# Optimization experiments

Hardware: AMD Instinct MI355X
Metric: run time of the kernel (lower is better)

The kernel has to match this reference:

```python
import jax, jax.numpy as jnp
import numpy as np

B, C, H, W = 4, 48, 512, 512

def gaussian_kernel(kernel_size, channels):
    # matches torch get_gaussian_kernel: sigma from OpenCV rule
    sigma = 0.3 * ((kernel_size - 1) * 0.5 - 1) + 0.8
    grid = np.arange(kernel_size, dtype=np.float32) - kernel_size // 2
    k1 = np.exp(-grid ** 2 / (2 * sigma ** 2))
    k1 /= k1.sum()
    k2 = np.outer(k1, k1)  # [k,k]
    # OIHW depthwise: [C, 1, k, k]
    return jnp.asarray(np.broadcast_to(k2, (channels, 1, kernel_size, kernel_size)))

def depthwise_conv(x, kernel, pad):
    # x: [B,C,H,W], kernel: [C,1,k,k]
    return jax.lax.conv_general_dilated(
        x, kernel,
        window_strides=(1, 1),
        padding=((pad, pad), (pad, pad)),
        dimension_numbers=('NCHW', 'OIHW', 'NCHW'),
        feature_group_count=x.shape[1])

def setup_inputs() -> dict:
    key = jax.random.key(0)
    s = jax.random.normal(key, (B, C, H, W), dtype=jnp.float32)
    one = jnp.ones((), dtype=jnp.float32)
    return {'s': s, 'w1': one, 'w2': one, 'w3': one, 'w4': one}

def reference(s, w1, w2, w3, w4):
    channels = s.shape[1]
    k3 = gaussian_kernel(3, channels)
    k5 = gaussian_kernel(5, channels)
    k7 = gaussian_kernel(7, channels)
    s3 = depthwise_conv(s, k3, 1)
    s5 = depthwise_conv(s, k5, 2)
    s7 = depthwise_conv(s, k7, 3)
    # fused diff + weighted sum: w1*s + w2*(s-s3) + w3*(s3-s5) + w4*(s5-s7)
    return w1 * s + w2 * (s - s3) + w3 * (s3 - s5) + w4 * (s5 - s7)
```

## Files before the change

### kernel.cpp

```cpp
#include <hip/hip_runtime.h>
#include <math.h>

#define STRIP_H 32

struct GaussCoefs { float g3[3]; float g5[5]; float g7[7]; };

__device__ __forceinline__ float rfl(float x) {
    return __int_as_float(__builtin_amdgcn_readfirstlane(__float_as_int(x)));
}

#define Z4 make_float4(0.f, 0.f, 0.f, 0.f)

#define ADD4(A, W, F) \
    A.x = fmaf((W), (F).x, A.x); A.y = fmaf((W), (F).y, A.y); \
    A.z = fmaf((W), (F).z, A.z); A.w = fmaf((W), (F).w, A.w);

#define DOT7(a,b,c,d,e,f,g) \
    fmaf(g7h0,(a), fmaf(g7h1,(b), fmaf(g7h2,(c), fmaf(g7h3,(d), \
    fmaf(g7h4,(e), fmaf(g7h5,(f), (g7h6)*(g)))))))
#define DOT5(a,b,c,d,e) \
    fmaf(g5h0,(a), fmaf(g5h1,(b), fmaf(g5h2,(c), fmaf(g5h3,(d), (g5h4)*(e)))))
#define DOT3(a,b,c) \
    fmaf(g3h0,(a), fmaf(g3h1,(b), (g3h2)*(c)))

#define LOADR(vA, vB, vC) \
    float4 vA, vB, vC; \
    if ((unsigned)row < (unsigned)Hd) { \
        const float* rp_ = sp + row * Wd; \
        vA = *(const float4*)(rp_ + offA); \
        vB = *(const float4*)(rp_ + offB); \
        vC = *(const float4*)(rp_ + offC); \
        if (killA) vA = Z4; \
        if (killC) vC = Z4; \
    } else { vA = Z4; vB = Z4; vC = Z4; } \
    ++row;

#define H7CALC(vA,vB,vC,h7) float4 h7; \
    h7.x = DOT7(vA.y,vA.z,vA.w,vB.x,vB.y,vB.z,vB.w); \
    h7.y = DOT7(vA.z,vA.w,vB.x,vB.y,vB.z,vB.w,vC.x); \
    h7.z = DOT7(vA.w,vB.x,vB.y,vB.z,vB.w,vC.x,vC.y); \
    h7.w = DOT7(vB.x,vB.y,vB.z,vB.w,vC.x,vC.y,vC.z);
#define H5CALC(vA,vB,vC,h5) float4 h5; \
    h5.x = DOT5(vA.z,vA.w,vB.x,vB.y,vB.z); \
    h5.y = DOT5(vA.w,vB.x,vB.y,vB.z,vB.w); \
    h5.z = DOT5(vB.x,vB.y,vB.z,vB.w,vC.x); \
    h5.w = DOT5(vB.y,vB.z,vB.w,vC.x,vC.y);
#define H3CALC(vA,vB,vC,h3) float4 h3; \
    h3.x = DOT3(vA.w,vB.x,vB.y); \
    h3.y = DOT3(vB.x,vB.y,vB.z); \
    h3.z = DOT3(vB.y,vB.z,vB.w); \
    h3.w = DOT3(vB.z,vB.w,vC.x);

#define MAINSTEP(S0,S1,S2,S3,S4,S5,S6) { \
    LOADR(vA, vB, vC); \
    H7CALC(vA,vB,vC,h7); H5CALC(vA,vB,vC,h5); H3CALC(vA,vB,vC,h3); \
    ADD4(S0, w7v6, h7); ADD4(S1, w7v5, h7); ADD4(S2, w7v4, h7); \
    ADD4(S3, w7v3, h7); ADD4(S4, w7v2, h7); ADD4(S5, w7v1, h7); \
    ADD4(S6, w7v0, h7); \
    ADD4(S1, w5v4, h5); ADD4(S2, w5v3, h5); ADD4(S3, w5v2, h5); \
    ADD4(S4, w5v1, h5); ADD4(S5, w5v0, h5); \
    ADD4(S2, w3v2, h3); ADD4(S3, w3v1, h3); ADD4(S4, w3v0, h3); \
    ADD4(S3, a0, vB); \
    *(float4*)(op + orow * Wd + xb) = S0; \
    S0 = Z4; ++orow; }

__global__ __launch_bounds__(256, 4) void mgdf_kernel(
    const float* __restrict__ s,
    const float* __restrict__ w1p, const float* __restrict__ w2p,
    const float* __restrict__ w3p, const float* __restrict__ w4p,
    float* __restrict__ out,
    GaussCoefs gc, int Wd, int Hd)
{
    const int tid  = threadIdx.x;
    const int lane = tid & 63;
    const int xh   = (tid >> 6) & 1;
    const int ysub = tid >> 7;
    const int plane = blockIdx.z;
    const int xb   = xh * 256 + lane * 4;
    const int ys0  = (blockIdx.y * 2 + ysub) * STRIP_H;

    const float* sp = s + (size_t)plane * Hd * Wd;
    float*       op = out + (size_t)plane * Hd * Wd;

    const float w1 = *w1p, w2 = *w2p, w3 = *w3p, w4 = *w4p;
    const float a0v = w1 + w2, a3v = w3 - w2, a5v = w4 - w3, a7v = -w4;

    const float g7h0 = gc.g7[0], g7h1 = gc.g7[1], g7h2 = gc.g7[2],
                g7h3 = gc.g7[3], g7h4 = gc.g7[4], g7h5 = gc.g7[5],
                g7h6 = gc.g7[6];
    const float g5h0 = gc.g5[0], g5h1 = gc.g5[1], g5h2 = gc.g5[2],
                g5h3 = gc.g5[3], g5h4 = gc.g5[4];
    const float g3h0 = gc.g3[0], g3h1 = gc.g3[1], g3h2 = gc.g3[2];

    const float a0   = rfl(a0v);
    const float w7v0 = rfl(a7v * g7h0), w7v1 = rfl(a7v * g7h1),
                w7v2 = rfl(a7v * g7h2), w7v3 = rfl(a7v * g7h3),
                w7v4 = rfl(a7v * g7h4), w7v5 = rfl(a7v * g7h5),
                w7v6 = rfl(a7v * g7h6);
    const float w5v0 = rfl(a5v * g5h0), w5v1 = rfl(a5v * g5h1),
                w5v2 = rfl(a5v * g5h2), w5v3 = rfl(a5v * g5h3),
                w5v4 = rfl(a5v * g5h4);
    const float w3v0 = rfl(a3v * g3h0), w3v1 = rfl(a3v * g3h1),
                w3v2 = rfl(a3v * g3h2);

    const bool killA = (xb - 4) < 0;
    const bool killC = (xb + 7) >= Wd;
    const int offA = killA ? xb : (xb - 4);
    const int offB = xb;
    const int offC = killC ? xb : (xb + 4);

    int row  = ys0 - 3;
    int orow = ys0;

    float4 A0 = Z4, A1 = Z4, A2 = Z4, A3 = Z4,
           A4 = Z4, A5 = Z4, A6 = Z4, A7 = Z4;

    { LOADR(vA,vB,vC); H7CALC(vA,vB,vC,h7);
      ADD4(A0, w7v0, h7); }
    { LOADR(vA,vB,vC); H7CALC(vA,vB,vC,h7); H5CALC(vA,vB,vC,h5);
      ADD4(A1, w7v0, h7); ADD4(A0, w7v1, h7);
      ADD4(A0, w5v0, h5); }
    { LOADR(vA,vB,vC); H7CALC(vA,vB,vC,h7); H5CALC(vA,vB,vC,h5); H3CALC(vA,vB,vC,h3);
      ADD4(A2, w7v0, h7); ADD4(A1, w7v1, h7); ADD4(A0, w7v2, h7);
      ADD4(A1, w5v0, h5); ADD4(A0, w5v1, h5);
      ADD4(A0, w3v0, h3); }
    { LOADR(vA,vB,vC); H7CALC(vA,vB,vC,h7); H5CALC(vA,vB,vC,h5); H3CALC(vA,vB,vC,h3);
      ADD4(A3, w7v0, h7); ADD4(A2, w7v1, h7); ADD4(A1, w7v2, h7); ADD4(A0, w7v3, h7);
      ADD4(A2, w5v0, h5); ADD4(A1, w5v1, h5); ADD4(A0, w5v2, h5);
      ADD4(A1, w3v0, h3); ADD4(A0, w3v1, h3);
      ADD4(A0, a0, vB); }
    { LOADR(vA,vB,vC); H7CALC(vA,vB,vC,h7); H5CALC(vA,vB,vC,h5); H3CALC(vA,vB,vC,h3);
      ADD4(A4, w7v0, h7); ADD4(A3, w7v1, h7); ADD4(A2, w7v2, h7);
      ADD4(A1, w7v3, h7); ADD4(A0, w7v4, h7);
      ADD4(A3, w5v0, h5); ADD4(A2, w5v1, h5); ADD4(A1, w5v2, h5); ADD4(A0, w5v3, h5);
      ADD4(A2, w3v0, h3); ADD4(A1, w3v1, h3); ADD4(A0, w3v2, h3);
      ADD4(A1, a0, vB); }
    { LOADR(vA,vB,vC); H7CALC(vA,vB,vC,h7); H5CALC(vA,vB,vC,h5); H3CALC(vA,vB,vC,h3);
      ADD4(A5, w7v0, h7); ADD4(A4, w7v1, h7); ADD4(A3, w7v2, h7);
      ADD4(A2, w7v3, h7); ADD4(A1, w7v4, h7); ADD4(A0, w7v5, h7);
      ADD4(A4, w5v0, h5); ADD4(A3, w5v1, h5); ADD4(A2, w5v2, h5);
      ADD4(A1, w5v3, h5); ADD4(A0, w5v4, h5);
      ADD4(A3, w3v0, h3); ADD4(A2, w3v1, h3); ADD4(A1, w3v2, h3);
      ADD4(A2, a0, vB); }

    #pragma unroll 1
    for (int it = 0; it < STRIP_H / 8; ++it) {
        MAINSTEP(A0, A1, A2, A3, A4, A5, A6);
        MAINSTEP(A1, A2, A3, A4, A5, A6, A7);
        MAINSTEP(A2, A3, A4, A5, A6, A7, A0);
        MAINSTEP(A3, A4, A5, A6, A7, A0, A1);
        MAINSTEP(A4, A5, A6, A7, A0, A1, A2);
        MAINSTEP(A5, A6, A7, A0, A1, A2, A3);
        MAINSTEP(A6, A7, A0, A1, A2, A3, A4);
        MAINSTEP(A7, A0, A1, A2, A3, A4, A5);
    }
}

static void fill_gauss(float* g, int k) {
    const double sigma = 0.3 * ((k - 1) * 0.5 - 1.0) + 0.8;
    double t[7], sum = 0.0;
    for (int i = 0; i < k; ++i) {
        const double x = (double)(i - k / 2);
        t[i] = exp(-x * x / (2.0 * sigma * sigma));
        sum += t[i];
    }
    for (int i = 0; i < k; ++i) g[i] = (float)(t[i] / sum);
}

extern "C" void kernel_launch(void* const* d_in, const int* in_sizes, int n_in,
                              void* d_out, int out_size, void* d_ws, size_t ws_size,
                              hipStream_t stream) {
    const float* s  = (const float*)d_in[0];
    const float* w1 = (const float*)d_in[1];
    const float* w2 = (const float*)d_in[2];
    const float* w3 = (const float*)d_in[3];
    const float* w4 = (const float*)d_in[4];
    float* out = (float*)d_out;

    const int Hd = 512, Wd = 512;
    const int planes = in_sizes[0] / (Hd * Wd);

    GaussCoefs gc;
    fill_gauss(gc.g3, 3);
    fill_gauss(gc.g5, 5);
    fill_gauss(gc.g7, 7);

    dim3 grid(1, Hd / (2 * STRIP_H), planes);
    mgdf_kernel<<<grid, 256, 0, stream>>>(s, w1, w2, w3, w4, out, gc, Wd, Hd);
}
```

Measured before the change: 370.2 us.

## Software-prefetch next row with double-buffered registers and halve strip height

Each step now issues the global loads for the next input row into a second set of registers before computing on the current row, so load latency can overlap with the filter arithmetic. The strip height is halved to 16 and the main loop is fully unrolled, which doubles the number of blocks and the share of halo rows reloaded per strip. The extra prefetch buffers raise register pressure under the 4-blocks-per-CU launch bound.

```diff
diff --git a/kernel.cpp b/kernel.cpp
--- a/kernel.cpp
+++ b/kernel.cpp
@@ -1,7 +1,7 @@
 #include <hip/hip_runtime.h>
 #include <math.h>
 
-#define STRIP_H 32
+#define STRIP_H 16
 
 struct GaussCoefs { float g3[3]; float g5[5]; float g7[7]; };
 
@@ -23,46 +23,64 @@
 #define DOT3(a,b,c) \
     fmaf(g3h0,(a), fmaf(g3h1,(b), (g3h2)*(c)))
 
-#define LOADR(vA, vB, vC) \
-    float4 vA, vB, vC; \
+#define PFLOAD(NA, NB, NC) \
     if ((unsigned)row < (unsigned)Hd) { \
-        const float* rp_ = sp + row * Wd; \
-        vA = *(const float4*)(rp_ + offA); \
-        vB = *(const float4*)(rp_ + offB); \
-        vC = *(const float4*)(rp_ + offC); \
-        if (killA) vA = Z4; \
-        if (killC) vC = Z4; \
-    } else { vA = Z4; vB = Z4; vC = Z4; } \
+        const float* rp_ = sp + (size_t)row * Wd; \
+        NA = *(const float4*)(rp_ + offA); \
+        NB = *(const float4*)(rp_ + offB); \
+        NC = *(const float4*)(rp_ + offC); \
+    } else { NA = Z4; NB = Z4; NC = Z4; } \
     ++row;
 
-#define H7CALC(vA,vB,vC,h7) float4 h7; \
-    h7.x = DOT7(vA.y,vA.z,vA.w,vB.x,vB.y,vB.z,vB.w); \
-    h7.y = DOT7(vA.z,vA.w,vB.x,vB.y,vB.z,vB.w,vC.x); \
-    h7.z = DOT7(vA.w,vB.x,vB.y,vB.z,vB.w,vC.x,vC.y); \
-    h7.w = DOT7(vB.x,vB.y,vB.z,vB.w,vC.x,vC.y,vC.z);
-#define H5CALC(vA,vB,vC,h5) float4 h5; \
-    h5.x = DOT5(vA.z,vA.w,vB.x,vB.y,vB.z); \
-    h5.y = DOT5(vA.w,vB.x,vB.y,vB.z,vB.w); \
-    h5.z = DOT5(vB.x,vB.y,vB.z,vB.w,vC.x); \
-    h5.w = DOT5(vB.y,vB.z,vB.w,vC.x,vC.y);
-#define H3CALC(vA,vB,vC,h3) float4 h3; \
-    h3.x = DOT3(vA.w,vB.x,vB.y); \
-    h3.y = DOT3(vB.x,vB.y,vB.z); \
-    h3.z = DOT3(vB.y,vB.z,vB.w); \
-    h3.w = DOT3(vB.z,vB.w,vC.x);
-
-#define MAINSTEP(S0,S1,S2,S3,S4,S5,S6) { \
-    LOADR(vA, vB, vC); \
-    H7CALC(vA,vB,vC,h7); H5CALC(vA,vB,vC,h5); H3CALC(vA,vB,vC,h3); \
+#define CSTEP(CA,CB,CC, NA,NB,NC, ...) { \
+    PFLOAD(NA, NB, NC); \
+    if (killA) CA = Z4; \
+    if (killC) CC = Z4; \
+    float4 h7, h5, h3; \
+    h7.x = DOT7(CA.y,CA.z,CA.w,CB.x,CB.y,CB.z,CB.w); \
+    h7.y = DOT7(CA.z,CA.w,CB.x,CB.y,CB.z,CB.w,CC.x); \
+    h7.z = DOT7(CA.w,CB.x,CB.y,CB.z,CB.w,CC.x,CC.y); \
+    h7.w = DOT7(CB.x,CB.y,CB.z,CB.w,CC.x,CC.y,CC.z); \
+    h5.x = DOT5(CA.z,CA.w,CB.x,CB.y,CB.z); \
+    h5.y = DOT5(CA.w,CB.x,CB.y,CB.z,CB.w); \
+    h5.z = DOT5(CB.x,CB.y,CB.z,CB.w,CC.x); \
+    h5.w = DOT5(CB.y,CB.z,CB.w,CC.x,CC.y); \
+    h3.x = DOT3(CA.w,CB.x,CB.y); \
+    h3.y = DOT3(CB.x,CB.y,CB.z); \
+    h3.z = DOT3(CB.y,CB.z,CB.w); \
+    h3.w = DOT3(CB.z,CB.w,CC.x); \
+    (void)h5; (void)h3; \
+    __VA_ARGS__ }
+
+#define CSTEP_LAST(CA,CB,CC, ...) { \
+    if (killA) CA = Z4; \
+    if (killC) CC = Z4; \
+    float4 h7, h5, h3; \
+    h7.x = DOT7(CA.y,CA.z,CA.w,CB.x,CB.y,CB.z,CB.w); \
+    h7.y = DOT7(CA.z,CA.w,CB.x,CB.y,CB.z,CB.w,CC.x); \
+    h7.z = DOT7(CA.w,CB.x,CB.y,CB.z,CB.w,CC.x,CC.y); \
+    h7.w = DOT7(CB.x,CB.y,CB.z,CB.w,CC.x,CC.y,CC.z); \
+    h5.x = DOT5(CA.z,CA.w,CB.x,CB.y,CB.z); \
+    h5.y = DOT5(CA.w,CB.x,CB.y,CB.z,CB.w); \
+    h5.z = DOT5(CB.x,CB.y,CB.z,CB.w,CC.x); \
+    h5.w = DOT5(CB.y,CB.z,CB.w,CC.x,CC.y); \
+    h3.x = DOT3(CA.w,CB.x,CB.y); \
+    h3.y = DOT3(CB.x,CB.y,CB.z); \
+    h3.z = DOT3(CB.y,CB.z,CB.w); \
+    h3.w = DOT3(CB.z,CB.w,CC.x); \
+    (void)h5; (void)h3; \
+    __VA_ARGS__ }
+
+#define MAINB(S0,S1,S2,S3,S4,S5,S6, CB) \
     ADD4(S0, w7v6, h7); ADD4(S1, w7v5, h7); ADD4(S2, w7v4, h7); \
     ADD4(S3, w7v3, h7); ADD4(S4, w7v2, h7); ADD4(S5, w7v1, h7); \
     ADD4(S6, w7v0, h7); \
     ADD4(S1, w5v4, h5); ADD4(S2, w5v3, h5); ADD4(S3, w5v2, h5); \
     ADD4(S4, w5v1, h5); ADD4(S5, w5v0, h5); \
     ADD4(S2, w3v2, h3); ADD4(S3, w3v1, h3); ADD4(S4, w3v0, h3); \
-    ADD4(S3, a0, vB); \
-    *(float4*)(op + orow * Wd + xb) = S0; \
-    S0 = Z4; ++orow; }
+    ADD4(S3, a0, CB); \
+    *(float4*)(op + (size_t)orow * Wd + xb) = S0; \
+    S0 = Z4; ++orow;
 
 __global__ __launch_bounds__(256, 4) void mgdf_kernel(
     const float* __restrict__ s,
@@ -114,46 +132,54 @@
 
     float4 A0 = Z4, A1 = Z4, A2 = Z4, A3 = Z4,
            A4 = Z4, A5 = Z4, A6 = Z4, A7 = Z4;
-
-    { LOADR(vA,vB,vC); H7CALC(vA,vB,vC,h7);
-      ADD4(A0, w7v0, h7); }
-    { LOADR(vA,vB,vC); H7CALC(vA,vB,vC,h7); H5CALC(vA,vB,vC,h5);
+    float4 p0a, p0b, p0c, p1a, p1b, p1c;
+
+    PFLOAD(p0a, p0b, p0c);
+
+    CSTEP(p0a,p0b,p0c, p1a,p1b,p1c,
+      ADD4(A0, w7v0, h7); )
+    CSTEP(p1a,p1b,p1c, p0a,p0b,p0c,
       ADD4(A1, w7v0, h7); ADD4(A0, w7v1, h7);
-      ADD4(A0, w5v0, h5); }
-    { LOADR(vA,vB,vC); H7CALC(vA,vB,vC,h7); H5CALC(vA,vB,vC,h5); H3CALC(vA,vB,vC,h3);
+      ADD4(A0, w5v0, h5); )
+    CSTEP(p0a,p0b,p0c, p1a,p1b,p1c,
       ADD4(A2, w7v0, h7); ADD4(A1, w7v1, h7); ADD4(A0, w7v2, h7);
       ADD4(A1, w5v0, h5); ADD4(A0, w5v1, h5);
-      ADD4(A0, w3v0, h3); }
-    { LOADR(vA,vB,vC); H7CALC(vA,vB,vC,h7); H5CALC(vA,vB,vC,h5); H3CALC(vA,vB,vC,h3);
+      ADD4(A0, w3v0, h3); )
+    CSTEP(p1a,p1b,p1c, p0a,p0b,p0c,
       ADD4(A3, w7v0, h7); ADD4(A2, w7v1, h7); ADD4(A1, w7v2, h7); ADD4(A0, w7v3, h7);
       ADD4(A2, w5v0, h5); ADD4(A1, w5v1, h5); ADD4(A0, w5v2, h5);
       ADD4(A1, w3v0, h3); ADD4(A0, w3v1, h3);
-      ADD4(A0, a0, vB); }
-    { LOADR(vA,vB,vC); H7CALC(vA,vB,vC,h7); H5CALC(vA,vB,vC,h5); H3CALC(vA,vB,vC,h3);
+      ADD4(A0, a0, p1b); )
+    CSTEP(p0a,p0b,p0c, p1a,p1b,p1c,
       ADD4(A4, w7v0, h7); ADD4(A3, w7v1, h7); ADD4(A2, w7v2, h7);
       ADD4(A1, w7v3, h7); ADD4(A0, w7v4, h7);
       ADD4(A3, w5v0, h5); ADD4(A2, w5v1, h5); ADD4(A1, w5v2, h5); ADD4(A0, w5v3, h5);
       ADD4(A2, w3v0, h3); ADD4(A1, w3v1, h3); ADD4(A0, w3v2, h3);
-      ADD4(A1, a0, vB); }
-    { LOADR(vA,vB,vC); H7CALC(vA,vB,vC,h7); H5CALC(vA,vB,vC,h5); H3CALC(vA,vB,vC,h3);
+      ADD4(A1, a0, p0b); )
+    CSTEP(p1a,p1b,p1c, p0a,p0b,p0c,
       ADD4(A5, w7v0, h7); ADD4(A4, w7v1, h7); ADD4(A3, w7v2, h7);
       ADD4(A2, w7v3, h7); ADD4(A1, w7v4, h7); ADD4(A0, w7v5, h7);
       ADD4(A4, w5v0, h5); ADD4(A3, w5v1, h5); ADD4(A2, w5v2, h5);
       ADD4(A1, w5v3, h5); ADD4(A0, w5v4, h5);
       ADD4(A3, w3v0, h3); ADD4(A2, w3v1, h3); ADD4(A1, w3v2, h3);
-      ADD4(A2, a0, vB); }
-
-    #pragma unroll 1
-    for (int it = 0; it < STRIP_H / 8; ++it) {
-        MAINSTEP(A0, A1, A2, A3, A4, A5, A6);
-        MAINSTEP(A1, A2, A3, A4, A5, A6, A7);
-        MAINSTEP(A2, A3, A4, A5, A6, A7, A0);
-        MAINSTEP(A3, A4, A5, A6, A7, A0, A1);
-        MAINSTEP(A4, A5, A6, A7, A0, A1, A2);
-        MAINSTEP(A5, A6, A7, A0, A1, A2, A3);
-        MAINSTEP(A6, A7, A0, A1, A2, A3, A4);
-        MAINSTEP(A7, A0, A1, A2, A3, A4, A5);
-    }
+      ADD4(A2, a0, p1b); )
+
+    CSTEP(p0a,p0b,p0c, p1a,p1b,p1c, MAINB(A0,A1,A2,A3,A4,A5,A6, p0b))
+    CSTEP(p1a,p1b,p1c, p0a,p0b,p0c, MAINB(A1,A2,A3,A4,A5,A6,A7, p1b))
+    CSTEP(p0a,p0b,p0c, p1a,p1b,p1c, MAINB(A2,A3,A4,A5,A6,A7,A0, p0b))
+    CSTEP(p1a,p1b,p1c, p0a,p0b,p0c, MAINB(A3,A4,A5,A6,A7,A0,A1, p1b))
+    CSTEP(p0a,p0b,p0c, p1a,p1b,p1c, MAINB(A4,A5,A6,A7,A0,A1,A2, p0b))
+    CSTEP(p1a,p1b,p1c, p0a,p0b,p0c, MAINB(A5,A6,A7,A0,A1,A2,A3, p1b))
+    CSTEP(p0a,p0b,p0c, p1a,p1b,p1c, MAINB(A6,A7,A0,A1,A2,A3,A4, p0b))
+    CSTEP(p1a,p1b,p1c, p0a,p0b,p0c, MAINB(A7,A0,A1,A2,A3,A4,A5, p1b))
+    CSTEP(p0a,p0b,p0c, p1a,p1b,p1c, MAINB(A0,A1,A2,A3,A4,A5,A6, p0b))
+    CSTEP(p1a,p1b,p1c, p0a,p0b,p0c, MAINB(A1,A2,A3,A4,A5,A6,A7, p1b))
+    CSTEP(p0a,p0b,p0c, p1a,p1b,p1c, MAINB(A2,A3,A4,A5,A6,A7,A0, p0b))
+    CSTEP(p1a,p1b,p1c, p0a,p0b,p0c, MAINB(A3,A4,A5,A6,A7,A0,A1, p1b))
+    CSTEP(p0a,p0b,p0c, p1a,p1b,p1c, MAINB(A4,A5,A6,A7,A0,A1,A2, p0b))
+    CSTEP(p1a,p1b,p1c, p0a,p0b,p0c, MAINB(A5,A6,A7,A0,A1,A2,A3, p1b))
+    CSTEP(p0a,p0b,p0c, p1a,p1b,p1c, MAINB(A6,A7,A0,A1,A2,A3,A4, p0b))
+    CSTEP_LAST(p1a,p1b,p1c,         MAINB(A7,A0,A1,A2,A3,A4,A5, p1b))
 }
 
 static void fill_gauss(float* g, int k) {
```

After: 344.1 us. 7.1% less time.
